# Performance work log

Measured on AMD Instinct MI355X. Metric: run time of the kernel, lower is better.

Reference implementation:

```python
import jax, jax.numpy as jnp
import numpy as np

DIM = 128
NUM_HEADS = 8


def setup_inputs() -> dict:
    key = jax.random.key(0)
    ks = jax.random.split(key, 5)
    B, L, C = 4, 16384, DIM
    x = jax.random.normal(ks[0], (B, L, C), dtype=jnp.float32)
    # Linear params (stored as (in, out) so y = x @ W + b)
    w_qkv = jax.random.normal(ks[1], (C, 3 * C), dtype=jnp.float32) * (C ** -0.5)
    b_qkv = jax.random.normal(ks[2], (3 * C,), dtype=jnp.float32) * 0.02
    w_proj = jax.random.normal(ks[3], (C, C), dtype=jnp.float32) * (C ** -0.5)
    b_proj = jax.random.normal(ks[4], (C,), dtype=jnp.float32) * 0.02
    return {"x": x, "w_qkv": w_qkv, "b_qkv": b_qkv, "w_proj": w_proj, "b_proj": b_proj}


def reference(x, w_qkv, b_qkv, w_proj, b_proj):
    B, L, C = x.shape
    H = NUM_HEADS
    hd = C // H
    scale = C ** -0.5  # note: torch code scales by dim**-0.5, not head_dim**-0.5

    qkv = x @ w_qkv + b_qkv                      # (B, L, 3C)
    q, k, v = jnp.split(qkv, 3, axis=-1)         # each (B, L, C)

    def to_heads(t):
        return t.reshape(B, L, H, hd).transpose(0, 2, 1, 3)  # (B, H, L, hd)

    q, k, v = to_heads(q), to_heads(k), to_heads(v)

    # Per-token outer product over head_dim: (B, H, L, hd, hd)
    attn = (q * scale)[..., :, None] * k[..., None, :]
    attn = jax.nn.softmax(attn, axis=-1)

    # attn @ v per token: (B, H, L, hd)
    out = jnp.einsum("bhlij,bhlj->bhli", attn, v)
    out = out.transpose(0, 2, 1, 3).reshape(B, L, C)  # (B, L, C)
    return out @ w_proj + b_proj
```

## Files before the change

kernel.cpp:

```cpp
#include <hip/hip_runtime.h>


typedef __attribute__((ext_vector_type(8))) short bf16x8;
typedef __attribute__((ext_vector_type(4))) float f32x4;
typedef __attribute__((ext_vector_type(4))) unsigned int u32x4;

#define TILE_M 32
#define QKV_STRIDE_F 388
#define O_STRIDE 136

__device__ __forceinline__ unsigned short f2bf(float f) {
    unsigned int u = __builtin_bit_cast(unsigned int, f);
    u += 0x8000u;
    return (unsigned short)(u >> 16);
}
__device__ __forceinline__ unsigned int pkbf(float lo, float hi) {
    unsigned int a = __builtin_bit_cast(unsigned int, lo) + 0x8000u;
    unsigned int b = __builtin_bit_cast(unsigned int, hi) + 0x8000u;
    return __builtin_amdgcn_perm(b, a, 0x07060302u);
}

__global__ void prep_weights(const float* __restrict__ wqkv,
                             const float* __restrict__ wproj,
                             unsigned short* __restrict__ wqkvT,
                             unsigned short* __restrict__ wprojT) {
    int idx = blockIdx.x * 256 + threadIdx.x;
    if (idx < 384 * 128) {
        int n = idx >> 7, k = idx & 127;
        wqkvT[idx] = f2bf(wqkv[k * 384 + n]);
    }
    if (idx < 128 * 128) {
        int n = idx >> 7, k = idx & 127;
        wprojT[idx] = f2bf(wproj[k * 128 + n]);
    }
}

__global__ __launch_bounds__(256, 3) void fused_channel_attn(
    const float* __restrict__ x,
    const unsigned short* __restrict__ wqkvT,
    const float* __restrict__ bqkv,
    const unsigned short* __restrict__ wprojT,
    const float* __restrict__ bproj,
    float* __restrict__ out)
{
    __shared__ __align__(16) float us_f[TILE_M * QKV_STRIDE_F];
    unsigned short* us_o = (unsigned short*)us_f;

    const int tid  = threadIdx.x;
    const int lane = tid & 63;
    const int wave = tid >> 6;
    const int col  = lane & 15;
    const int quad = lane >> 4;
    const long base_tok = (long)blockIdx.x * TILE_M;

    const int nb = wave * 6;

    float4 xf[2][4][2];
#pragma unroll
    for (int m = 0; m < 2; ++m) {
        const float* xrow = x + (base_tok + m * 16 + col) * 128;
#pragma unroll
        for (int ks = 0; ks < 4; ++ks) {
            const float4* p = (const float4*)(xrow + ks * 32 + quad * 8);
            xf[m][ks][0] = p[0];
            xf[m][ks][1] = p[1];
        }
    }
    bf16x8 afr[2][4];
#pragma unroll
    for (int m = 0; m < 2; ++m)
#pragma unroll
        for (int ks = 0; ks < 4; ++ks) {
            float4 f0 = xf[m][ks][0], f1 = xf[m][ks][1];
            u32x4 a = {pkbf(f0.x, f0.y), pkbf(f0.z, f0.w),
                       pkbf(f1.x, f1.y), pkbf(f1.z, f1.w)};
            afr[m][ks] = __builtin_bit_cast(bf16x8, a);
        }

    f32x4 acc[2][6];
#pragma unroll
    for (int j = 0; j < 6; ++j) {
        float b = bqkv[(nb + j) * 16 + col];
        acc[0][j] = (f32x4){b, b, b, b};
        acc[1][j] = (f32x4){b, b, b, b};
    }
#pragma unroll
    for (int ks = 0; ks < 4; ++ks) {
        bf16x8 bfr[6];
#pragma unroll
        for (int j = 0; j < 6; ++j)
            bfr[j] = *(const bf16x8*)&wqkvT[((nb + j) * 16 + col) * 128 + ks * 32 + quad * 8];
#pragma unroll
        for (int j = 0; j < 6; ++j) {
            acc[0][j] = __builtin_amdgcn_mfma_f32_16x16x32_bf16(afr[0][ks], bfr[j], acc[0][j], 0, 0, 0);
            acc[1][j] = __builtin_amdgcn_mfma_f32_16x16x32_bf16(afr[1][ks], bfr[j], acc[1][j], 0, 0, 0);
        }
    }

#pragma unroll
    for (int m = 0; m < 2; ++m)
#pragma unroll
        for (int j = 0; j < 6; ++j)
#pragma unroll
            for (int r = 0; r < 4; ++r)
                us_f[(m * 16 + quad * 4 + r) * QKV_STRIDE_F + (nb + j) * 16 + col] = acc[m][j][r];
    __syncthreads();

    const int t = tid & 31;
    const int h = tid >> 5;
    const float* qkvrow = us_f + t * QKV_STRIDE_F + h * 16;

    float4 qv4[4], kv4[4], vv4[4];
#pragma unroll
    for (int c = 0; c < 4; ++c) {
        qv4[c] = ((const float4*)(qkvrow))[c];
        kv4[c] = ((const float4*)(qkvrow + 128))[c];
        vv4[c] = ((const float4*)(qkvrow + 256))[c];
    }
    __syncthreads();

    const float sl2e = 0.08838834764831845f * 1.44269504088896340f;
    float qv[16], kf[16], vf[16];
#pragma unroll
    for (int c = 0; c < 4; ++c) {
        qv[4*c] = qv4[c].x; qv[4*c+1] = qv4[c].y; qv[4*c+2] = qv4[c].z; qv[4*c+3] = qv4[c].w;
        kf[4*c] = kv4[c].x; kf[4*c+1] = kv4[c].y; kf[4*c+2] = kv4[c].z; kf[4*c+3] = kv4[c].w;
        vf[4*c] = vv4[c].x; vf[4*c+1] = vv4[c].y; vf[4*c+2] = vv4[c].z; vf[4*c+3] = vv4[c].w;
    }
    float ov[16];
#pragma unroll
    for (int i = 0; i < 16; ++i) {
        float qs = qv[i] * sl2e;
        float den = 0.f, num = 0.f;
#pragma unroll
        for (int j = 0; j < 16; ++j) {
            float e = __builtin_amdgcn_exp2f(qs * kf[j]);
            den += e;
            num = fmaf(e, vf[j], num);
        }
        ov[i] = num * __builtin_amdgcn_rcpf(den);
    }
    u32x4 o0 = {pkbf(ov[0], ov[1]), pkbf(ov[2], ov[3]), pkbf(ov[4], ov[5]), pkbf(ov[6], ov[7])};
    u32x4 o1 = {pkbf(ov[8], ov[9]), pkbf(ov[10], ov[11]), pkbf(ov[12], ov[13]), pkbf(ov[14], ov[15])};
    *(u32x4*)&us_o[t * O_STRIDE + h * 16]     = o0;
    *(u32x4*)&us_o[t * O_STRIDE + h * 16 + 8] = o1;
    __syncthreads();

    const int nb2 = wave * 2;
    bf16x8 af2[2][4];
#pragma unroll
    for (int m = 0; m < 2; ++m)
#pragma unroll
        for (int ks = 0; ks < 4; ++ks)
            af2[m][ks] = *(const bf16x8*)&us_o[(m * 16 + col) * O_STRIDE + ks * 32 + quad * 8];

    f32x4 acc2[2][2];
#pragma unroll
    for (int n = 0; n < 2; ++n) {
        float b = bproj[(nb2 + n) * 16 + col];
        acc2[0][n] = (f32x4){b, b, b, b};
        acc2[1][n] = (f32x4){b, b, b, b};
    }
#pragma unroll
    for (int ks = 0; ks < 4; ++ks) {
        bf16x8 bb[2];
#pragma unroll
        for (int n = 0; n < 2; ++n)
            bb[n] = *(const bf16x8*)&wprojT[((nb2 + n) * 16 + col) * 128 + ks * 32 + quad * 8];
#pragma unroll
        for (int n = 0; n < 2; ++n) {
            acc2[0][n] = __builtin_amdgcn_mfma_f32_16x16x32_bf16(af2[0][ks], bb[n], acc2[0][n], 0, 0, 0);
            acc2[1][n] = __builtin_amdgcn_mfma_f32_16x16x32_bf16(af2[1][ks], bb[n], acc2[1][n], 0, 0, 0);
        }
    }
#pragma unroll
    for (int m = 0; m < 2; ++m)
#pragma unroll
        for (int n = 0; n < 2; ++n)
#pragma unroll
            for (int r = 0; r < 4; ++r) {
                long tt = base_tok + m * 16 + quad * 4 + r;
                out[tt * 128 + (nb2 + n) * 16 + col] = acc2[m][n][r];
            }
}

extern "C" void kernel_launch(void* const* d_in, const int* in_sizes, int n_in,
                              void* d_out, int out_size, void* d_ws, size_t ws_size,
                              hipStream_t stream) {
    const float* x     = (const float*)d_in[0];
    const float* wqkv  = (const float*)d_in[1];
    const float* bqkv  = (const float*)d_in[2];
    const float* wproj = (const float*)d_in[3];
    const float* bproj = (const float*)d_in[4];
    float* out = (float*)d_out;

    unsigned short* wqkvT  = (unsigned short*)d_ws;
    unsigned short* wprojT = wqkvT + 384 * 128;

    prep_weights<<<192, 256, 0, stream>>>(wqkv, wproj, wqkvT, wprojT);

    const int tokens = in_sizes[0] / 128;
    fused_channel_attn<<<tokens / TILE_M, 256, 0, stream>>>(
        x, wqkvT, bqkv, wprojT, bproj, out);
}
```

Measured before the change: 131.7 us.

## Store QKV tile as bf16 in LDS and raise occupancy target

After: 169.6 us. 1.29x slower.

```diff
diff --git a/kernel.cpp b/kernel.cpp
--- a/kernel.cpp
+++ b/kernel.cpp
@@ -6,7 +6,7 @@
 typedef __attribute__((ext_vector_type(4))) unsigned int u32x4;
 
 #define TILE_M 32
-#define QKV_STRIDE_F 388
+#define QKV_STRIDE 392
 #define O_STRIDE 136
 
 __device__ __forceinline__ unsigned short f2bf(float f) {
@@ -18,6 +18,12 @@
     unsigned int a = __builtin_bit_cast(unsigned int, lo) + 0x8000u;
     unsigned int b = __builtin_bit_cast(unsigned int, hi) + 0x8000u;
     return __builtin_amdgcn_perm(b, a, 0x07060302u);
+}
+__device__ __forceinline__ float bflo(unsigned int u) {
+    return __builtin_bit_cast(float, u << 16);
+}
+__device__ __forceinline__ float bfhi(unsigned int u) {
+    return __builtin_bit_cast(float, u & 0xffff0000u);
 }
 
 __global__ void prep_weights(const float* __restrict__ wqkv,
@@ -35,7 +41,7 @@
     }
 }
 
-__global__ __launch_bounds__(256, 3) void fused_channel_attn(
+__global__ __launch_bounds__(256, 6) void fused_channel_attn(
     const float* __restrict__ x,
     const unsigned short* __restrict__ wqkvT,
     const float* __restrict__ bqkv,
@@ -43,8 +49,7 @@
     const float* __restrict__ bproj,
     float* __restrict__ out)
 {
-    __shared__ __align__(16) float us_f[TILE_M * QKV_STRIDE_F];
-    unsigned short* us_o = (unsigned short*)us_f;
+    __shared__ __align__(16) unsigned short us[TILE_M * QKV_STRIDE];
 
     const int tid  = threadIdx.x;
     const int lane = tid & 63;
@@ -55,27 +60,25 @@
 
     const int nb = wave * 6;
 
-    float4 xf[2][4][2];
+    bf16x8 afr[2][4];
 #pragma unroll
     for (int m = 0; m < 2; ++m) {
         const float* xrow = x + (base_tok + m * 16 + col) * 128;
+        float4 s[4][2];
 #pragma unroll
         for (int ks = 0; ks < 4; ++ks) {
             const float4* p = (const float4*)(xrow + ks * 32 + quad * 8);
-            xf[m][ks][0] = p[0];
-            xf[m][ks][1] = p[1];
-        }
-    }
-    bf16x8 afr[2][4];
-#pragma unroll
-    for (int m = 0; m < 2; ++m)
+            s[ks][0] = p[0];
+            s[ks][1] = p[1];
+        }
 #pragma unroll
         for (int ks = 0; ks < 4; ++ks) {
-            float4 f0 = xf[m][ks][0], f1 = xf[m][ks][1];
+            float4 f0 = s[ks][0], f1 = s[ks][1];
             u32x4 a = {pkbf(f0.x, f0.y), pkbf(f0.z, f0.w),
                        pkbf(f1.x, f1.y), pkbf(f1.z, f1.w)};
             afr[m][ks] = __builtin_bit_cast(bf16x8, a);
         }
+    }
 
     f32x4 acc[2][6];
 #pragma unroll
@@ -86,46 +89,52 @@
     }
 #pragma unroll
     for (int ks = 0; ks < 4; ++ks) {
-        bf16x8 bfr[6];
+#pragma unroll
+        for (int half = 0; half < 2; ++half) {
+            bf16x8 bfr[3];
+#pragma unroll
+            for (int j = 0; j < 3; ++j)
+                bfr[j] = *(const bf16x8*)&wqkvT[((nb + half * 3 + j) * 16 + col) * 128 + ks * 32 + quad * 8];
+#pragma unroll
+            for (int j = 0; j < 3; ++j) {
+                int jj = half * 3 + j;
+                acc[0][jj] = __builtin_amdgcn_mfma_f32_16x16x32_bf16(afr[0][ks], bfr[j], acc[0][jj], 0, 0, 0);
+                acc[1][jj] = __builtin_amdgcn_mfma_f32_16x16x32_bf16(afr[1][ks], bfr[j], acc[1][jj], 0, 0, 0);
+            }
+        }
+    }
+
+#pragma unroll
+    for (int m = 0; m < 2; ++m)
 #pragma unroll
         for (int j = 0; j < 6; ++j)
-            bfr[j] = *(const bf16x8*)&wqkvT[((nb + j) * 16 + col) * 128 + ks * 32 + quad * 8];
-#pragma unroll
-        for (int j = 0; j < 6; ++j) {
-            acc[0][j] = __builtin_amdgcn_mfma_f32_16x16x32_bf16(afr[0][ks], bfr[j], acc[0][j], 0, 0, 0);
-            acc[1][j] = __builtin_amdgcn_mfma_f32_16x16x32_bf16(afr[1][ks], bfr[j], acc[1][j], 0, 0, 0);
-        }
-    }
-
-#pragma unroll
-    for (int m = 0; m < 2; ++m)
-#pragma unroll
-        for (int j = 0; j < 6; ++j)
 #pragma unroll
             for (int r = 0; r < 4; ++r)
-                us_f[(m * 16 + quad * 4 + r) * QKV_STRIDE_F + (nb + j) * 16 + col] = acc[m][j][r];
+                us[(m * 16 + quad * 4 + r) * QKV_STRIDE + (nb + j) * 16 + col] = f2bf(acc[m][j][r]);
     __syncthreads();
 
     const int t = tid & 31;
     const int h = tid >> 5;
-    const float* qkvrow = us_f + t * QKV_STRIDE_F + h * 16;
-
-    float4 qv4[4], kv4[4], vv4[4];
-#pragma unroll
-    for (int c = 0; c < 4; ++c) {
-        qv4[c] = ((const float4*)(qkvrow))[c];
-        kv4[c] = ((const float4*)(qkvrow + 128))[c];
-        vv4[c] = ((const float4*)(qkvrow + 256))[c];
-    }
+    const unsigned short* row = us + t * QKV_STRIDE + h * 16;
+
+    u32x4 qp0 = *(const u32x4*)(row);
+    u32x4 qp1 = *(const u32x4*)(row + 8);
+    u32x4 kp0 = *(const u32x4*)(row + 128);
+    u32x4 kp1 = *(const u32x4*)(row + 136);
+    u32x4 vp0 = *(const u32x4*)(row + 256);
+    u32x4 vp1 = *(const u32x4*)(row + 264);
     __syncthreads();
 
     const float sl2e = 0.08838834764831845f * 1.44269504088896340f;
     float qv[16], kf[16], vf[16];
 #pragma unroll
     for (int c = 0; c < 4; ++c) {
-        qv[4*c] = qv4[c].x; qv[4*c+1] = qv4[c].y; qv[4*c+2] = qv4[c].z; qv[4*c+3] = qv4[c].w;
-        kf[4*c] = kv4[c].x; kf[4*c+1] = kv4[c].y; kf[4*c+2] = kv4[c].z; kf[4*c+3] = kv4[c].w;
-        vf[4*c] = vv4[c].x; vf[4*c+1] = vv4[c].y; vf[4*c+2] = vv4[c].z; vf[4*c+3] = vv4[c].w;
+        qv[2*c]     = bflo(qp0[c]); qv[2*c+1]     = bfhi(qp0[c]);
+        qv[8+2*c]   = bflo(qp1[c]); qv[8+2*c+1]   = bfhi(qp1[c]);
+        kf[2*c]     = bflo(kp0[c]); kf[2*c+1]     = bfhi(kp0[c]);
+        kf[8+2*c]   = bflo(kp1[c]); kf[8+2*c+1]   = bfhi(kp1[c]);
+        vf[2*c]     = bflo(vp0[c]); vf[2*c+1]     = bfhi(vp0[c]);
+        vf[8+2*c]   = bflo(vp1[c]); vf[8+2*c+1]   = bfhi(vp1[c]);
     }
     float ov[16];
 #pragma unroll
@@ -142,8 +151,8 @@
     }
     u32x4 o0 = {pkbf(ov[0], ov[1]), pkbf(ov[2], ov[3]), pkbf(ov[4], ov[5]), pkbf(ov[6], ov[7])};
     u32x4 o1 = {pkbf(ov[8], ov[9]), pkbf(ov[10], ov[11]), pkbf(ov[12], ov[13]), pkbf(ov[14], ov[15])};
-    *(u32x4*)&us_o[t * O_STRIDE + h * 16]     = o0;
-    *(u32x4*)&us_o[t * O_STRIDE + h * 16 + 8] = o1;
+    *(u32x4*)&us[t * O_STRIDE + h * 16]     = o0;
+    *(u32x4*)&us[t * O_STRIDE + h * 16 + 8] = o1;
     __syncthreads();
 
     const int nb2 = wave * 2;
@@ -152,7 +161,7 @@
     for (int m = 0; m < 2; ++m)
 #pragma unroll
         for (int ks = 0; ks < 4; ++ks)
-            af2[m][ks] = *(const bf16x8*)&us_o[(m * 16 + col) * O_STRIDE + ks * 32 + quad * 8];
+            af2[m][ks] = *(const bf16x8*)&us[(m * 16 + col) * O_STRIDE + ks * 32 + quad * 8];
 
     f32x4 acc2[2][2];
 #pragma unroll
```
